# Performance work log

Hardware: AMD Instinct MI355X
Metric: run time of the kernel (lower is better)

## Reference

```python
import jax, jax.numpy as jnp
import numpy as np

B, S, D, H, DFF, HID = 512, 100, 512, 2, 256, 230
DH = D // H


def _ln_torch(x, g, b, eps=1e-5):
    # nn.LayerNorm: biased variance, eps inside sqrt
    m = x.mean(-1, keepdims=True)
    v = ((x - m) ** 2).mean(-1, keepdims=True)
    return g * (x - m) / jnp.sqrt(v + eps) + b


def _ln_custom(x, g, b, eps=1e-6):
    # repo's custom LayerNorm: unbiased std (torch.std default), eps added to std
    m = x.mean(-1, keepdims=True)
    s = jnp.std(x, axis=-1, ddof=1, keepdims=True)
    return g * (x - m) / (s + eps) + b


def setup_inputs() -> dict:
    key = jax.random.key(0)
    ks = jax.random.split(key, 32)
    w = lambda k, shape: jax.random.normal(k, shape, jnp.float32) * 0.02
    return {
        'inp': jax.random.normal(ks[0], (B, S, D), jnp.float32),
        'mask': jax.random.randint(ks[1], (B, S), 0, 2).astype(jnp.int32),
        'gate': jax.random.uniform(ks[2], (B, S, S), jnp.float32),
        'wv': w(ks[3], (D, D)), 'bv': jnp.zeros((D,), jnp.float32),
        'fc_w': w(ks[4], (D, D)), 'fc_b': jnp.zeros((D,), jnp.float32),
        'lnm_g': jnp.ones((D,), jnp.float32), 'lnm_b': jnp.zeros((D,), jnp.float32),
        'w1': w(ks[5], (DFF, D)), 'b1': jnp.zeros((DFF,), jnp.float32),
        'w2': w(ks[6], (D, DFF)), 'b2': jnp.zeros((D,), jnp.float32),
        'lpc_w': w(ks[7], (D, D)), 'lpc_b': jnp.zeros((D,), jnp.float32),
        'lnc_g': jnp.ones((D,), jnp.float32), 'lnc_b': jnp.zeros((D,), jnp.float32),
        'pwf_w': w(ks[8], (DFF, D)), 'pwf_b': jnp.zeros((DFF,), jnp.float32),
        'lpi_w': w(ks[9], (D, DFF)), 'lpi_b': jnp.zeros((D,), jnp.float32),
        'lni_g': jnp.ones((D,), jnp.float32), 'lni_b': jnp.zeros((D,), jnp.float32),
        'lnf_g': jnp.ones((D,), jnp.float32), 'lnf_b': jnp.zeros((D,), jnp.float32),
        'mlpf_w': w(ks[10], (HID, D)), 'mlpf_b': jnp.zeros((HID,), jnp.float32),
    }


def reference(inp, mask, gate, wv, bv, fc_w, fc_b, lnm_g, lnm_b, w1, b1, w2, b2,
              lpc_w, lpc_b, lnc_g, lnc_b, pwf_w, pwf_b, lpi_w, lpi_b,
              lni_g, lni_b, lnf_g, lnf_b, mlpf_w, mlpf_b):
    b = inp.shape[0]
    maskf = mask.astype(jnp.float32)
    masks = maskf[:, :, None] * maskf[:, None, :]              # [B,S,S]
    # In the source, attention scores are FULLY replaced by the mask via
    # torch.where(mask==0, 1e-8, mask); the q/k projections and the gate
    # multiplication have no effect on the output (dead computation).
    attn = jnp.where(masks == 0, jnp.float32(1e-8), masks)
    p = jax.nn.softmax(attn, axis=-1)                          # [B,S,S] (same for both heads)
    v = (inp @ wv.T + bv).reshape(b, S, H, DH)                 # [B,S,H,dh]
    ctx = jnp.einsum('bst,bthd->bshd', p, v).reshape(b, S, D)  # head-concat order matches torch
    mha = _ln_torch(ctx @ fc_w.T + fc_b + inp, lnm_g, lnm_b)   # dropout = identity (eval)
    # 1x1-conv FFN + custom LN
    ffn = jax.nn.relu(mha @ w1.T + b1) @ w2.T + b2
    ctx2 = _ln_custom(ffn + mha, lni_g, lni_b)
    # context projection applied to BOTH original inp and ffn output (shared weights)
    res_inp = _ln_custom((inp @ lpc_w.T + lpc_b) + (ctx2 @ lpc_w.T + lpc_b), lnc_g, lnc_b)
    rv = jax.nn.relu(res_inp @ pwf_w.T + pwf_b) @ lpi_w.T + lpi_b
    res = _ln_custom(rv + res_inp, lnf_g, lnf_b)
    return res @ mlpf_w.T + mlpf_b                             # x_for_att: [B,S,230]
```

## Files before the change

kernel.cpp:

```cpp
#include <hip/hip_runtime.h>

#define BB  512
#define SS  100
#define DD  512
#define DFF 256
#define HIDN 230
#define LDA 520

typedef unsigned short u16;
typedef unsigned int   u32;
typedef __attribute__((ext_vector_type(8))) short v8s;
typedef __attribute__((ext_vector_type(4))) float v4f;

__device__ __forceinline__ float b2f(u16 u){
  union { u32 i; float f; } v; v.i = ((u32)u) << 16; return v.f;
}
__device__ __forceinline__ u16 f2b(float f){
  union { float f; u32 i; } v; v.f = f;
  u32 r = (v.i + 0x7fffu + ((v.i >> 16) & 1u)) >> 16;
  return (u16)r;
}
__device__ __forceinline__ float rsum16(float s){
  #pragma unroll
  for (int o = 1; o < 16; o <<= 1) s += __shfl_xor(s, o, 64);
  return s;
}

template<int K, int NJ>
__device__ __forceinline__ void mm_2m(const u16* __restrict__ a0r,
                                      const u16* __restrict__ a1r,
                                      const u16* __restrict__ b0,
                                      v4f (*acc)[NJ]){
  constexpr int NC = K / 32;
  v8s b[NJ];
  #pragma unroll
  for (int j = 0; j < NJ; j++) b[j] = *(const v8s*)(b0 + (size_t)j*128*K);
  v8s a0 = *(const v8s*)(a0r);
  v8s a1 = *(const v8s*)(a1r);
  #pragma unroll
  for (int kc = 0; kc < NC; kc++){
    v8s bn[NJ]; v8s a0n, a1n;
    if (kc + 1 < NC){
      #pragma unroll
      for (int j = 0; j < NJ; j++)
        bn[j] = *(const v8s*)(b0 + (size_t)j*128*K + (kc+1)*512);
      a0n = *(const v8s*)(a0r + (kc+1)*32);
      a1n = *(const v8s*)(a1r + (kc+1)*32);
    } else {
      #pragma unroll
      for (int j = 0; j < NJ; j++) bn[j] = b[j];
      a0n = a0; a1n = a1;
    }
    #pragma unroll
    for (int j = 0; j < NJ; j++){
      acc[0][j] = __builtin_amdgcn_mfma_f32_16x16x32_bf16(a0, b[j], acc[0][j], 0, 0, 0);
      acc[1][j] = __builtin_amdgcn_mfma_f32_16x16x32_bf16(a1, b[j], acc[1][j], 0, 0, 0);
    }
    #pragma unroll
    for (int j = 0; j < NJ; j++) b[j] = bn[j];
    a0 = a0n; a1 = a1n;
  }
}

template<bool ADDX>
__device__ __forceinline__ void ln_custom_pass(int lrow, int lc,
    const u16 (*src)[LDA], u16 (*dst)[LDA], const u32* xp,
    const u16* __restrict__ g, const u16* __restrict__ bb)
{
  float v[32]; float s = 0.f;
  #pragma unroll
  for (int j = 0; j < 32; j++){ int col = lc + j*16; float x = b2f(src[lrow][col]); v[j] = x; s += x; }
  s = rsum16(s);
  float mean = s * (1.0f/512.0f);
  float vs = 0.f;
  #pragma unroll
  for (int j = 0; j < 32; j++){ float d = v[j] - mean; vs += d*d; }
  vs = rsum16(vs);
  float inv = 1.0f / (sqrtf(vs * (1.0f/511.0f)) + 1e-6f);
  #pragma unroll
  for (int j = 0; j < 32; j++){
    int col = lc + j*16;
    float r = b2f(g[col]) * (v[j] - mean) * inv + b2f(bb[col]);
    if (ADDX){
      u32 p = xp[j >> 1];
      u16 xu = (j & 1) ? (u16)(p >> 16) : (u16)(p & 0xffffu);
      r += b2f(xu);
    }
    dst[lrow][col] = f2b(r);
  }
}

#define NSEG 20
struct CvtArgs {
  const float* src[NSEG];
  u16* dst;
  int off[NSEG];
  int n[NSEG];
  int ncs[6];
  int nin[6];
};
__global__ __launch_bounds__(256) void k_cvt(CvtArgs a){
  int total = a.off[NSEG-1] + a.n[NSEG-1];
  for (int i = blockIdx.x*blockDim.x + threadIdx.x; i < total; i += gridDim.x*blockDim.x){
    int s = 0;
    #pragma unroll
    for (int j = 1; j < NSEG; j++) if (i >= a.off[j]) s = j;
    int o = i - a.off[s];
    if (s < 6){
      int j  = o & 7;
      int l  = (o >> 3) & 63;
      int m  = l & 15, q = l >> 4;
      int rest = o >> 9;
      int ncs = a.ncs[s];
      int kc = rest & ((1 << ncs) - 1);
      int t  = rest >> ncs;
      int col = t*16 + m;
      int k   = kc*32 + q*8 + j;
      int K   = 32 << ncs;
      float v = (col < a.nin[s]) ? a.src[s][(size_t)col*K + k] : 0.f;
      a.dst[i] = f2b(v);
    } else {
      a.dst[i] = f2b(a.src[s][o]);
    }
  }
}

__global__ __launch_bounds__(512) void k_batch(
    const float* __restrict__ inp, const int* __restrict__ mask,
    const float* __restrict__ wv, const float* __restrict__ bv,
    const float* __restrict__ fcw, const float* __restrict__ fcb,
    float* __restrict__ a_m, float* __restrict__ a_u)
{
  __shared__ float sia[DD], sim[DD], cm[DD], cu[DD];
  __shared__ int smask[SS];
  const int b = blockIdx.x, t = threadIdx.x;
  const int lane = t & 63, w8 = t >> 6;
  if (t < SS) smask[t] = mask[b*SS + t];
  __syncthreads();
  const float* base = inp + (size_t)b * SS * DD;
  float aa = 0.f, am = 0.f; int n = 0;
  for (int s = 0; s < SS; s++){
    float x = base[s*DD + t];
    int mk = smask[s];
    aa += x; n += (mk != 0); if (mk) am += x;
  }
  sia[t] = aa; sim[t] = am;
  __syncthreads();
  const float e0 = expf(1e-8f - 1.0f);
  const float denom = (float)n + (float)(SS - n) * e0;
  const float p1 = 1.0f / denom, p0 = e0 / denom;
  {
    float s_a[8], s_m[8];
    #pragma unroll
    for (int j = 0; j < 8; j++){ s_a[j] = sia[lane*8 + j]; s_m[j] = sim[lane*8 + j]; }
    for (int rr = 0; rr < 64; rr++){
      int d = w8*64 + rr;
      const float4* wr = (const float4*)(wv + (size_t)d * DD + lane*8);
      float4 wA = wr[0], wB = wr[1];
      float sva = wA.x*s_a[0] + wA.y*s_a[1] + wA.z*s_a[2] + wA.w*s_a[3]
                + wB.x*s_a[4] + wB.y*s_a[5] + wB.z*s_a[6] + wB.w*s_a[7];
      float svm = wA.x*s_m[0] + wA.y*s_m[1] + wA.z*s_m[2] + wA.w*s_m[3]
                + wB.x*s_m[4] + wB.y*s_m[5] + wB.z*s_m[6] + wB.w*s_m[7];
      #pragma unroll
      for (int o = 1; o < 64; o <<= 1){ sva += __shfl_xor(sva, o, 64); svm += __shfl_xor(svm, o, 64); }
      if (lane == 0){
        float bvd = bv[d];
        sva += (float)SS * bvd;
        svm += (float)n  * bvd;
        cm[d] = p1*svm + p0*(sva - svm);
        cu[d] = sva * (1.0f/(float)SS);
      }
    }
  }
  __syncthreads();
  {
    float c_m[8], c_u[8];
    #pragma unroll
    for (int j = 0; j < 8; j++){ c_m[j] = cm[lane*8 + j]; c_u[j] = cu[lane*8 + j]; }
    for (int rr = 0; rr < 64; rr++){
      int d = w8*64 + rr;
      const float4* fr = (const float4*)(fcw + (size_t)d * DD + lane*8);
      float4 wA = fr[0], wB = fr[1];
      float xm = wA.x*c_m[0] + wA.y*c_m[1] + wA.z*c_m[2] + wA.w*c_m[3]
               + wB.x*c_m[4] + wB.y*c_m[5] + wB.z*c_m[6] + wB.w*c_m[7];
      float xu = wA.x*c_u[0] + wA.y*c_u[1] + wA.z*c_u[2] + wA.w*c_u[3]
               + wB.x*c_u[4] + wB.y*c_u[5] + wB.z*c_u[6] + wB.w*c_u[7];
      #pragma unroll
      for (int o = 1; o < 64; o <<= 1){ xm += __shfl_xor(xm, o, 64); xu += __shfl_xor(xu, o, 64); }
      if (lane == 0){
        float fb = fcb[d];
        a_m[(size_t)b*DD + d] = xm + fb;
        a_u[(size_t)b*DD + d] = xu + fb;
      }
    }
  }
}

__global__ __launch_bounds__(512, 4) void k_main(
    const float* __restrict__ inp, const int* __restrict__ mask,
    const u16* __restrict__ lnm_g, const u16* __restrict__ lnm_b,
    const u16* __restrict__ w1,   const u16* __restrict__ b1,
    const u16* __restrict__ w2,   const u16* __restrict__ b2,
    const u16* __restrict__ lpc_w, const u16* __restrict__ lpc_b,
    const u16* __restrict__ lnc_g, const u16* __restrict__ lnc_b,
    const u16* __restrict__ pwf_w, const u16* __restrict__ pwf_b,
    const u16* __restrict__ lpi_w, const u16* __restrict__ lpi_b,
    const u16* __restrict__ lni_g, const u16* __restrict__ lni_b,
    const u16* __restrict__ lnf_g, const u16* __restrict__ lnf_b,
    const u16* __restrict__ mlpf_w, const u16* __restrict__ mlpf_b,
    const float* __restrict__ a_m, const float* __restrict__ a_u,
    float* __restrict__ out)
{
  __shared__ __align__(16) u16 A[32][LDA];
  __shared__ __align__(16) u16 O[32][LDA];
  __shared__ int marr[32];

  const int tid  = threadIdx.x;
  const int lane = tid & 63, wid = tid >> 6;
  const int m = lane & 15, q = lane >> 4;
  const int r0 = blockIdx.x * 32;
  const int lrow = tid >> 4, lc = tid & 15;

  {
    if (tid < 32) marr[tid] = mask[r0 + tid];
    float4 va[4], vb[4];
    #pragma unroll
    for (int c = 0; c < 4; c++){
      int e = c*4096 + tid*8;
      int row = e >> 9, col = e & 511;
      const float4* p = (const float4*)(inp + (size_t)(r0 + row) * DD + col);
      va[c] = p[0]; vb[c] = p[1];
    }
    #pragma unroll
    for (int c = 0; c < 4; c++){
      int e = c*4096 + tid*8;
      int row = e >> 9, col = e & 511;
      uint4 o;
      o.x = (u32)f2b(va[c].x) | ((u32)f2b(va[c].y) << 16);
      o.y = (u32)f2b(va[c].z) | ((u32)f2b(va[c].w) << 16);
      o.z = (u32)f2b(vb[c].x) | ((u32)f2b(vb[c].y) << 16);
      o.w = (u32)f2b(vb[c].z) | ((u32)f2b(vb[c].w) << 16);
      *(uint4*)&O[row][col] = o;
    }
  }
  __syncthreads();

  u32 xp[16];
  {
    int Rg = r0 + lrow;
    int bi = Rg / SS;
    const float* asel = (marr[lrow] ? a_m : a_u) + (size_t)bi * DD;
    float v[32]; float s = 0.f;
    #pragma unroll
    for (int j = 0; j < 32; j++){
      int col = lc + j*16;
      u16 xu = O[lrow][col];
      if ((j & 1) == 0) xp[j >> 1] = (u32)xu;
      else              xp[j >> 1] |= ((u32)xu << 16);
      float x = asel[col] + b2f(xu);
      v[j] = x; s += x;
    }
    s = rsum16(s);
    float mean = s * (1.0f/512.0f);
    float vs = 0.f;
    #pragma unroll
    for (int j = 0; j < 32; j++){ float d = v[j] - mean; vs += d*d; }
    vs = rsum16(vs);
    float inv = 1.0f / sqrtf(vs * (1.0f/512.0f) + 1e-5f);
    #pragma unroll
    for (int j = 0; j < 32; j++){
      int col = lc + j*16;
      float r = b2f(lnm_g[col]) * (v[j] - mean) * inv + b2f(lnm_b[col]);
      A[lrow][col] = f2b(r);
    }
  }
  __syncthreads();

  {
    v4f acc[2][2];
    #pragma unroll
    for (int mt = 0; mt < 2; mt++)
      #pragma unroll
      for (int j = 0; j < 2; j++) acc[mt][j] = (v4f){0.f,0.f,0.f,0.f};
    mm_2m<512,2>(&A[m][q*8], &A[m+16][q*8], w1 + (size_t)wid*16*512 + lane*8, acc);
    #pragma unroll
    for (int j = 0; j < 2; j++){
      int col = (wid + 8*j)*16 + m;
      float bias = b2f(b1[col]);
      #pragma unroll
      for (int mt = 0; mt < 2; mt++)
        #pragma unroll
        for (int i = 0; i < 4; i++){
          float val = acc[mt][j][i] + bias;
          O[mt*16 + q*4 + i][col] = f2b(val > 0.f ? val : 0.f);
        }
    }
  }
  __syncthreads();

  {
    v4f acc[2][4];
    #pragma unroll
    for (int mt = 0; mt < 2; mt++)
      #pragma unroll
      for (int j = 0; j < 4; j++) acc[mt][j] = (v4f){0.f,0.f,0.f,0.f};
    mm_2m<256,4>(&O[m][q*8], &O[m+16][q*8], w2 + (size_t)wid*16*256 + lane*8, acc);
    __syncthreads();
    #pragma unroll
    for (int j = 0; j < 4; j++){
      int col = (wid + 8*j)*16 + m;
      float bias = b2f(b2[col]);
      #pragma unroll
      for (int mt = 0; mt < 2; mt++)
        #pragma unroll
        for (int i = 0; i < 4; i++){
          int row = mt*16 + q*4 + i;
          O[row][col] = f2b(acc[mt][j][i] + bias + b2f(A[row][col]));
        }
    }
  }
  __syncthreads();

  ln_custom_pass<true>(lrow, lc, O, A, xp, lni_g, lni_b);
  __syncthreads();

  {
    v4f acc[2][4];
    #pragma unroll
    for (int mt = 0; mt < 2; mt++)
      #pragma unroll
      for (int j = 0; j < 4; j++) acc[mt][j] = (v4f){0.f,0.f,0.f,0.f};
    mm_2m<512,4>(&A[m][q*8], &A[m+16][q*8], lpc_w + (size_t)wid*16*512 + lane*8, acc);
    #pragma unroll
    for (int j = 0; j < 4; j++){
      int col = (wid + 8*j)*16 + m;
      float bias = 2.0f * b2f(lpc_b[col]);
      #pragma unroll
      for (int mt = 0; mt < 2; mt++)
        #pragma unroll
        for (int i = 0; i < 4; i++) O[mt*16 + q*4 + i][col] = f2b(acc[mt][j][i] + bias);
    }
  }
  __syncthreads();

  ln_custom_pass<false>(lrow, lc, O, A, nullptr, lnc_g, lnc_b);
  __syncthreads();

  {
    v4f acc[2][2];
    #pragma unroll
    for (int mt = 0; mt < 2; mt++)
      #pragma unroll
      for (int j = 0; j < 2; j++) acc[mt][j] = (v4f){0.f,0.f,0.f,0.f};
    mm_2m<512,2>(&A[m][q*8], &A[m+16][q*8], pwf_w + (size_t)wid*16*512 + lane*8, acc);
    #pragma unroll
    for (int j = 0; j < 2; j++){
      int col = (wid + 8*j)*16 + m;
      float bias = b2f(pwf_b[col]);
      #pragma unroll
      for (int mt = 0; mt < 2; mt++)
        #pragma unroll
        for (int i = 0; i < 4; i++){
          float val = acc[mt][j][i] + bias;
          O[mt*16 + q*4 + i][col] = f2b(val > 0.f ? val : 0.f);
        }
    }
  }
  __syncthreads();

  {
    v4f acc[2][4];
    #pragma unroll
    for (int mt = 0; mt < 2; mt++)
      #pragma unroll
      for (int j = 0; j < 4; j++) acc[mt][j] = (v4f){0.f,0.f,0.f,0.f};
    mm_2m<256,4>(&O[m][q*8], &O[m+16][q*8], lpi_w + (size_t)wid*16*256 + lane*8, acc);
    __syncthreads();
    #pragma unroll
    for (int j = 0; j < 4; j++){
      int col = (wid + 8*j)*16 + m;
      float bias = b2f(lpi_b[col]);
      #pragma unroll
      for (int mt = 0; mt < 2; mt++)
        #pragma unroll
        for (int i = 0; i < 4; i++){
          int row = mt*16 + q*4 + i;
          O[row][col] = f2b(acc[mt][j][i] + bias + b2f(A[row][col]));
        }
    }
  }
  __syncthreads();

  ln_custom_pass<false>(lrow, lc, O, A, nullptr, lnf_g, lnf_b);
  __syncthreads();

  {
    v4f acc[2][2];
    #pragma unroll
    for (int mt = 0; mt < 2; mt++)
      #pragma unroll
      for (int j = 0; j < 2; j++) acc[mt][j] = (v4f){0.f,0.f,0.f,0.f};
    mm_2m<512,2>(&A[m][q*8], &A[m+16][q*8], mlpf_w + (size_t)wid*16*512 + lane*8, acc);
    #pragma unroll
    for (int j = 0; j < 2; j++){
      int col = (wid + 8*j)*16 + m;
      if (col < HIDN){
        float bias = b2f(mlpf_b[col]);
        #pragma unroll
        for (int mt = 0; mt < 2; mt++)
          #pragma unroll
          for (int i = 0; i < 4; i++){
            int row = mt*16 + q*4 + i;
            out[(size_t)(r0 + row)*HIDN + col] = acc[mt][j][i] + bias;
          }
      }
    }
  }
}

extern "C" void kernel_launch(void* const* d_in, const int* in_sizes, int n_in,
                              void* d_out, int out_size, void* d_ws, size_t ws_size,
                              hipStream_t stream)
{
  const float* inp    = (const float*)d_in[0];
  const int*   mask   = (const int*)d_in[1];
  const float* wv     = (const float*)d_in[3];
  const float* bv     = (const float*)d_in[4];
  const float* fc_w   = (const float*)d_in[5];
  const float* fc_b   = (const float*)d_in[6];

  float* a_m = (float*)d_ws;
  float* a_u = a_m + (size_t)BB * DD;
  u16* bfb = (u16*)((char*)d_ws + 2u * BB * DD * sizeof(float));

  const int OW1   = 0;
  const int OW2   = OW1   + DFF*DD;
  const int OLPC  = OW2   + DD*DFF;
  const int OPWF  = OLPC  + DD*DD;
  const int OLPI  = OPWF  + DFF*DD;
  const int OMLPF = OLPI  + DD*DFF;
  int voff = OMLPF + 256*DD;
  const int OLNMG = voff; voff += DD;
  const int OLNMB = voff; voff += DD;
  const int OB1   = voff; voff += DFF;
  const int OB2   = voff; voff += DD;
  const int OLPCB = voff; voff += DD;
  const int OLNCG = voff; voff += DD;
  const int OLNCB = voff; voff += DD;
  const int OPWFB = voff; voff += DFF;
  const int OLPIB = voff; voff += DD;
  const int OLNIG = voff; voff += DD;
  const int OLNIB = voff; voff += DD;
  const int OLNFG = voff; voff += DD;
  const int OLNFB = voff; voff += DD;
  const int OMLPFB = voff; voff += HIDN;

  CvtArgs ca;
  const int srcidx[NSEG] = {9, 11, 13, 17, 19, 25,
                            7, 8, 10, 12, 14, 15, 16, 18, 20, 21, 22, 23, 24, 26};
  const int offs[NSEG]   = {OW1, OW2, OLPC, OPWF, OLPI, OMLPF,
                            OLNMG, OLNMB, OB1, OB2, OLPCB, OLNCG, OLNCB, OPWFB,
                            OLPIB, OLNIG, OLNIB, OLNFG, OLNFB, OMLPFB};
  const int lens[NSEG]   = {DFF*DD, DD*DFF, DD*DD, DFF*DD, DD*DFF, 256*DD,
                            DD, DD, DFF, DD, DD, DD, DD, DFF, DD, DD, DD, DD, DD, HIDN};
  const int ncss[6] = {4, 3, 4, 4, 3, 4};
  const int nins[6] = {DFF, DD, DD, DFF, DD, HIDN};
  for (int i = 0; i < NSEG; i++){
    ca.src[i] = (const float*)d_in[srcidx[i]];
    ca.off[i] = offs[i];
    ca.n[i]   = lens[i];
  }
  for (int i = 0; i < 6; i++){ ca.ncs[i] = ncss[i]; ca.nin[i] = nins[i]; }
  ca.dst = bfb;

  k_cvt<<<512, 256, 0, stream>>>(ca);
  k_batch<<<BB, 512, 0, stream>>>(inp, mask, wv, bv, fc_w, fc_b, a_m, a_u);
  k_main<<<(BB*SS)/32, 512, 0, stream>>>(inp, mask,
      bfb + OLNMG, bfb + OLNMB,
      bfb + OW1,   bfb + OB1,
      bfb + OW2,   bfb + OB2,
      bfb + OLPC,  bfb + OLPCB,
      bfb + OLNCG, bfb + OLNCB,
      bfb + OPWF,  bfb + OPWFB,
      bfb + OLPI,  bfb + OLPIB,
      bfb + OLNIG, bfb + OLNIB,
      bfb + OLNFG, bfb + OLNFB,
      bfb + OMLPF, bfb + OMLPFB,
      a_m, a_u, (float*)d_out);
}
```

Before: 588.0 us.

## Process 64 rows per block with 16 waves and fuse conversion into prep kernel

New measurement: 540.3 us. -8.1%, faster.

```diff
diff --git a/kernel.cpp b/kernel.cpp
--- a/kernel.cpp
+++ b/kernel.cpp
@@ -26,39 +26,41 @@
   return s;
 }
 
-template<int K, int NJ>
-__device__ __forceinline__ void mm_2m(const u16* __restrict__ a0r,
-                                      const u16* __restrict__ a1r,
-                                      const u16* __restrict__ b0,
-                                      v4f (*acc)[NJ]){
+template<int K, int NT>
+__device__ __forceinline__ void mm64(const u16 (*Asrc)[LDA], const u16* __restrict__ W,
+                                     int w, int lane, int m, int q, v4f (*acc)[NT]){
   constexpr int NC = K / 32;
-  v8s b[NJ];
-  #pragma unroll
-  for (int j = 0; j < NJ; j++) b[j] = *(const v8s*)(b0 + (size_t)j*128*K);
-  v8s a0 = *(const v8s*)(a0r);
-  v8s a1 = *(const v8s*)(a1r);
+  const u16* b0 = W + (size_t)w*16*K + lane*8;
+  v8s a[4], b[NT];
+  #pragma unroll
+  for (int mt = 0; mt < 4; mt++) a[mt] = *(const v8s*)(&Asrc[mt*16 + m][q*8]);
+  #pragma unroll
+  for (int j = 0; j < NT; j++)  b[j]  = *(const v8s*)(b0 + (size_t)j*256*K);
   #pragma unroll
   for (int kc = 0; kc < NC; kc++){
-    v8s bn[NJ]; v8s a0n, a1n;
+    v8s an[4], bn[NT];
     if (kc + 1 < NC){
       #pragma unroll
-      for (int j = 0; j < NJ; j++)
-        bn[j] = *(const v8s*)(b0 + (size_t)j*128*K + (kc+1)*512);
-      a0n = *(const v8s*)(a0r + (kc+1)*32);
-      a1n = *(const v8s*)(a1r + (kc+1)*32);
+      for (int j = 0; j < NT; j++)
+        bn[j] = *(const v8s*)(b0 + (size_t)j*256*K + (kc+1)*512);
+      #pragma unroll
+      for (int mt = 0; mt < 4; mt++)
+        an[mt] = *(const v8s*)(&Asrc[mt*16 + m][(kc+1)*32 + q*8]);
     } else {
       #pragma unroll
-      for (int j = 0; j < NJ; j++) bn[j] = b[j];
-      a0n = a0; a1n = a1;
-    }
-    #pragma unroll
-    for (int j = 0; j < NJ; j++){
-      acc[0][j] = __builtin_amdgcn_mfma_f32_16x16x32_bf16(a0, b[j], acc[0][j], 0, 0, 0);
-      acc[1][j] = __builtin_amdgcn_mfma_f32_16x16x32_bf16(a1, b[j], acc[1][j], 0, 0, 0);
-    }
-    #pragma unroll
-    for (int j = 0; j < NJ; j++) b[j] = bn[j];
-    a0 = a0n; a1 = a1n;
+      for (int j = 0; j < NT; j++) bn[j] = b[j];
+      #pragma unroll
+      for (int mt = 0; mt < 4; mt++) an[mt] = a[mt];
+    }
+    #pragma unroll
+    for (int j = 0; j < NT; j++)
+      #pragma unroll
+      for (int mt = 0; mt < 4; mt++)
+        acc[mt][j] = __builtin_amdgcn_mfma_f32_16x16x32_bf16(a[mt], b[j], acc[mt][j], 0, 0, 0);
+    #pragma unroll
+    for (int j = 0; j < NT; j++) b[j] = bn[j];
+    #pragma unroll
+    for (int mt = 0; mt < 4; mt++) a[mt] = an[mt];
   }
 }
 
@@ -99,38 +101,37 @@
   int ncs[6];
   int nin[6];
 };
-__global__ __launch_bounds__(256) void k_cvt(CvtArgs a){
-  int total = a.off[NSEG-1] + a.n[NSEG-1];
-  for (int i = blockIdx.x*blockDim.x + threadIdx.x; i < total; i += gridDim.x*blockDim.x){
-    int s = 0;
-    #pragma unroll
-    for (int j = 1; j < NSEG; j++) if (i >= a.off[j]) s = j;
-    int o = i - a.off[s];
-    if (s < 6){
-      int j  = o & 7;
-      int l  = (o >> 3) & 63;
-      int m  = l & 15, q = l >> 4;
-      int rest = o >> 9;
-      int ncs = a.ncs[s];
-      int kc = rest & ((1 << ncs) - 1);
-      int t  = rest >> ncs;
-      int col = t*16 + m;
-      int k   = kc*32 + q*8 + j;
-      int K   = 32 << ncs;
-      float v = (col < a.nin[s]) ? a.src[s][(size_t)col*K + k] : 0.f;
-      a.dst[i] = f2b(v);
-    } else {
-      a.dst[i] = f2b(a.src[s][o]);
-    }
-  }
-}
-
-__global__ __launch_bounds__(512) void k_batch(
+__global__ __launch_bounds__(512) void k_pre(CvtArgs a,
     const float* __restrict__ inp, const int* __restrict__ mask,
     const float* __restrict__ wv, const float* __restrict__ bv,
     const float* __restrict__ fcw, const float* __restrict__ fcb,
     float* __restrict__ a_m, float* __restrict__ a_u)
 {
+  {
+    int total = a.off[NSEG-1] + a.n[NSEG-1];
+    for (int i = blockIdx.x*blockDim.x + threadIdx.x; i < total; i += gridDim.x*blockDim.x){
+      int s = 0;
+      #pragma unroll
+      for (int j = 1; j < NSEG; j++) if (i >= a.off[j]) s = j;
+      int o = i - a.off[s];
+      if (s < 6){
+        int j  = o & 7;
+        int l  = (o >> 3) & 63;
+        int m  = l & 15, q = l >> 4;
+        int rest = o >> 9;
+        int ncs = a.ncs[s];
+        int kc = rest & ((1 << ncs) - 1);
+        int t  = rest >> ncs;
+        int col = t*16 + m;
+        int k   = kc*32 + q*8 + j;
+        int K   = 32 << ncs;
+        float v = (col < a.nin[s]) ? a.src[s][(size_t)col*K + k] : 0.f;
+        a.dst[i] = f2b(v);
+      } else {
+        a.dst[i] = f2b(a.src[s][o]);
+      }
+    }
+  }
   __shared__ float sia[DD], sim[DD], cm[DD], cu[DD];
   __shared__ int smask[SS];
   const int b = blockIdx.x, t = threadIdx.x;
@@ -196,7 +197,7 @@
   }
 }
 
-__global__ __launch_bounds__(512, 4) void k_main(
+__global__ __launch_bounds__(1024, 4) void k_main(
     const float* __restrict__ inp, const int* __restrict__ mask,
     const u16* __restrict__ lnm_g, const u16* __restrict__ lnm_b,
     const u16* __restrict__ w1,   const u16* __restrict__ b1,
@@ -211,29 +212,29 @@
     const float* __restrict__ a_m, const float* __restrict__ a_u,
     float* __restrict__ out)
 {
-  __shared__ __align__(16) u16 A[32][LDA];
-  __shared__ __align__(16) u16 O[32][LDA];
-  __shared__ int marr[32];
+  __shared__ __align__(16) u16 A[64][LDA];
+  __shared__ __align__(16) u16 O[64][LDA];
+  __shared__ int marr[64];
 
   const int tid  = threadIdx.x;
   const int lane = tid & 63, wid = tid >> 6;
   const int m = lane & 15, q = lane >> 4;
-  const int r0 = blockIdx.x * 32;
+  const int r0 = blockIdx.x * 64;
   const int lrow = tid >> 4, lc = tid & 15;
 
   {
-    if (tid < 32) marr[tid] = mask[r0 + tid];
+    if (tid < 64) marr[tid] = mask[r0 + tid];
     float4 va[4], vb[4];
     #pragma unroll
     for (int c = 0; c < 4; c++){
-      int e = c*4096 + tid*8;
+      int e = c*8192 + tid*8;
       int row = e >> 9, col = e & 511;
       const float4* p = (const float4*)(inp + (size_t)(r0 + row) * DD + col);
       va[c] = p[0]; vb[c] = p[1];
     }
     #pragma unroll
     for (int c = 0; c < 4; c++){
-      int e = c*4096 + tid*8;
+      int e = c*8192 + tid*8;
       int row = e >> 9, col = e & 511;
       uint4 o;
       o.x = (u32)f2b(va[c].x) | ((u32)f2b(va[c].y) << 16);
@@ -277,41 +278,36 @@
   __syncthreads();
 
   {
-    v4f acc[2][2];
-    #pragma unroll
-    for (int mt = 0; mt < 2; mt++)
+    v4f acc[4][1];
+    #pragma unroll
+    for (int mt = 0; mt < 4; mt++) acc[mt][0] = (v4f){0.f,0.f,0.f,0.f};
+    mm64<512,1>(A, w1, wid, lane, m, q, acc);
+    int col = wid*16 + m;
+    float bias = b2f(b1[col]);
+    #pragma unroll
+    for (int mt = 0; mt < 4; mt++)
+      #pragma unroll
+      for (int i = 0; i < 4; i++){
+        float val = acc[mt][0][i] + bias;
+        O[mt*16 + q*4 + i][col] = f2b(val > 0.f ? val : 0.f);
+      }
+  }
+  __syncthreads();
+
+  {
+    v4f acc[4][2];
+    #pragma unroll
+    for (int mt = 0; mt < 4; mt++)
       #pragma unroll
       for (int j = 0; j < 2; j++) acc[mt][j] = (v4f){0.f,0.f,0.f,0.f};
-    mm_2m<512,2>(&A[m][q*8], &A[m+16][q*8], w1 + (size_t)wid*16*512 + lane*8, acc);
+    mm64<256,2>(O, w2, wid, lane, m, q, acc);
+    __syncthreads();
     #pragma unroll
     for (int j = 0; j < 2; j++){
-      int col = (wid + 8*j)*16 + m;
-      float bias = b2f(b1[col]);
-      #pragma unroll
-      for (int mt = 0; mt < 2; mt++)
-        #pragma unroll
-        for (int i = 0; i < 4; i++){
-          float val = acc[mt][j][i] + bias;
-          O[mt*16 + q*4 + i][col] = f2b(val > 0.f ? val : 0.f);
-        }
-    }
-  }
-  __syncthreads();
-
-  {
-    v4f acc[2][4];
-    #pragma unroll
-    for (int mt = 0; mt < 2; mt++)
-      #pragma unroll
-      for (int j = 0; j < 4; j++) acc[mt][j] = (v4f){0.f,0.f,0.f,0.f};
-    mm_2m<256,4>(&O[m][q*8], &O[m+16][q*8], w2 + (size_t)wid*16*256 + lane*8, acc);
-    __syncthreads();
-    #pragma unroll
-    for (int j = 0; j < 4; j++){
-      int col = (wid + 8*j)*16 + m;
+      int col = (wid + 16*j)*16 + m;
       float bias = b2f(b2[col]);
       #pragma unroll
-      for (int mt = 0; mt < 2; mt++)
+      for (int mt = 0; mt < 4; mt++)
         #pragma unroll
         for (int i = 0; i < 4; i++){
           int row = mt*16 + q*4 + i;
@@ -325,18 +321,18 @@
   __syncthreads();
 
   {
-    v4f acc[2][4];
-    #pragma unroll
-    for (int mt = 0; mt < 2; mt++)
-      #pragma unroll
-      for (int j = 0; j < 4; j++) acc[mt][j] = (v4f){0.f,0.f,0.f,0.f};
-    mm_2m<512,4>(&A[m][q*8], &A[m+16][q*8], lpc_w + (size_t)wid*16*512 + lane*8, acc);
-    #pragma unroll
-    for (int j = 0; j < 4; j++){
-      int col = (wid + 8*j)*16 + m;
+    v4f acc[4][2];
+    #pragma unroll
+    for (int mt = 0; mt < 4; mt++)
+      #pragma unroll
+      for (int j = 0; j < 2; j++) acc[mt][j] = (v4f){0.f,0.f,0.f,0.f};
+    mm64<512,2>(A, lpc_w, wid, lane, m, q, acc);
+    #pragma unroll
+    for (int j = 0; j < 2; j++){
+      int col = (wid + 16*j)*16 + m;
       float bias = 2.0f * b2f(lpc_b[col]);
       #pragma unroll
-      for (int mt = 0; mt < 2; mt++)
+      for (int mt = 0; mt < 4; mt++)
         #pragma unroll
         for (int i = 0; i < 4; i++) O[mt*16 + q*4 + i][col] = f2b(acc[mt][j][i] + bias);
     }
@@ -347,41 +343,36 @@
   __syncthreads();
 
   {
-    v4f acc[2][2];
-    #pragma unroll
-    for (int mt = 0; mt < 2; mt++)
+    v4f acc[4][1];
+    #pragma unroll
+    for (int mt = 0; mt < 4; mt++) acc[mt][0] = (v4f){0.f,0.f,0.f,0.f};
+    mm64<512,1>(A, pwf_w, wid, lane, m, q, acc);
+    int col = wid*16 + m;
+    float bias = b2f(pwf_b[col]);
+    #pragma unroll
+    for (int mt = 0; mt < 4; mt++)
+      #pragma unroll
+      for (int i = 0; i < 4; i++){
+        float val = acc[mt][0][i] + bias;
+        O[mt*16 + q*4 + i][col] = f2b(val > 0.f ? val : 0.f);
+      }
+  }
+  __syncthreads();
+
+  {
+    v4f acc[4][2];
+    #pragma unroll
+    for (int mt = 0; mt < 4; mt++)
       #pragma unroll
       for (int j = 0; j < 2; j++) acc[mt][j] = (v4f){0.f,0.f,0.f,0.f};
-    mm_2m<512,2>(&A[m][q*8], &A[m+16][q*8], pwf_w + (size_t)wid*16*512 + lane*8, acc);
+    mm64<256,2>(O, lpi_w, wid, lane, m, q, acc);
+    __syncthreads();
     #pragma unroll
     for (int j = 0; j < 2; j++){
-      int col = (wid + 8*j)*16 + m;
-      float bias = b2f(pwf_b[col]);
-      #pragma unroll
-      for (int mt = 0; mt < 2; mt++)
-        #pragma unroll
-        for (int i = 0; i < 4; i++){
-          float val = acc[mt][j][i] + bias;
-          O[mt*16 + q*4 + i][col] = f2b(val > 0.f ? val : 0.f);
-        }
-    }
-  }
-  __syncthreads();
-
-  {
-    v4f acc[2][4];
-    #pragma unroll
-    for (int mt = 0; mt < 2; mt++)
-      #pragma unroll
-      for (int j = 0; j < 4; j++) acc[mt][j] = (v4f){0.f,0.f,0.f,0.f};
-    mm_2m<256,4>(&O[m][q*8], &O[m+16][q*8], lpi_w + (size_t)wid*16*256 + lane*8, acc);
-    __syncthreads();
-    #pragma unroll
-    for (int j = 0; j < 4; j++){
-      int col = (wid + 8*j)*16 + m;
+      int col = (wid + 16*j)*16 + m;
       float bias = b2f(lpi_b[col]);
       #pragma unroll
-      for (int mt = 0; mt < 2; mt++)
+      for (int mt = 0; mt < 4; mt++)
         #pragma unroll
         for (int i = 0; i < 4; i++){
           int row = mt*16 + q*4 + i;
@@ -395,25 +386,20 @@
   __syncthreads();
 
   {
-    v4f acc[2][2];
-    #pragma unroll
-    for (int mt = 0; mt < 2; mt++)
-      #pragma unroll
-      for (int j = 0; j < 2; j++) acc[mt][j] = (v4f){0.f,0.f,0.f,0.f};
-    mm_2m<512,2>(&A[m][q*8], &A[m+16][q*8], mlpf_w + (size_t)wid*16*512 + lane*8, acc);
-    #pragma unroll
-    for (int j = 0; j < 2; j++){
-      int col = (wid + 8*j)*16 + m;
-      if (col < HIDN){
-        float bias = b2f(mlpf_b[col]);
+    v4f acc[4][1];
+    #pragma unroll
+    for (int mt = 0; mt < 4; mt++) acc[mt][0] = (v4f){0.f,0.f,0.f,0.f};
+    mm64<512,1>(A, mlpf_w, wid, lane, m, q, acc);
+    int col = wid*16 + m;
+    if (col < HIDN){
+      float bias = b2f(mlpf_b[col]);
+      #pragma unroll
+      for (int mt = 0; mt < 4; mt++)
         #pragma unroll
-        for (int mt = 0; mt < 2; mt++)
-          #pragma unroll
-          for (int i = 0; i < 4; i++){
-            int row = mt*16 + q*4 + i;
-            out[(size_t)(r0 + row)*HIDN + col] = acc[mt][j][i] + bias;
-          }
-      }
+        for (int i = 0; i < 4; i++){
+          int row = mt*16 + q*4 + i;
+          out[(size_t)(r0 + row)*HIDN + col] = acc[mt][0][i] + bias;
+        }
     }
   }
 }
@@ -473,9 +459,8 @@
   for (int i = 0; i < 6; i++){ ca.ncs[i] = ncss[i]; ca.nin[i] = nins[i]; }
   ca.dst = bfb;
 
-  k_cvt<<<512, 256, 0, stream>>>(ca);
-  k_batch<<<BB, 512, 0, stream>>>(inp, mask, wv, bv, fc_w, fc_b, a_m, a_u);
-  k_main<<<(BB*SS)/32, 512, 0, stream>>>(inp, mask,
+  k_pre<<<BB, 512, 0, stream>>>(ca, inp, mask, wv, bv, fc_w, fc_b, a_m, a_u);
+  k_main<<<(BB*SS)/64, 1024, 0, stream>>>(inp, mask,
       bfb + OLNMG, bfb + OLNMB,
       bfb + OW1,   bfb + OB1,
       bfb + OW2,   bfb + OB2,
```

## Merge conversion into batch kernel and shrink shared memory with in-place LN buffers

Applied to the files above, without the earlier changes.

After: 577.0 us. Within noise of the previous version (-1.9%).

```diff
diff --git a/kernel.cpp b/kernel.cpp
--- a/kernel.cpp
+++ b/kernel.cpp
@@ -6,6 +6,7 @@
 #define DFF 256
 #define HIDN 230
 #define LDA 520
+#define LDB 264
 
 typedef unsigned short u16;
 typedef unsigned int   u32;
@@ -26,50 +27,52 @@
   return s;
 }
 
-template<int K, int NJ>
-__device__ __forceinline__ void mm_2m(const u16* __restrict__ a0r,
-                                      const u16* __restrict__ a1r,
-                                      const u16* __restrict__ b0,
-                                      v4f (*acc)[NJ]){
+template<int K, int NT, int LDAS>
+__device__ __forceinline__ void mmW(const u16 (*Asrc)[LDAS], const u16* __restrict__ W,
+                                    int w, int lane, int m, int q, v4f (*acc)[NT]){
   constexpr int NC = K / 32;
-  v8s b[NJ];
-  #pragma unroll
-  for (int j = 0; j < NJ; j++) b[j] = *(const v8s*)(b0 + (size_t)j*128*K);
-  v8s a0 = *(const v8s*)(a0r);
-  v8s a1 = *(const v8s*)(a1r);
+  const u16* b0 = W + (size_t)w*16*K + lane*8;
+  v8s a[2], b[NT];
+  #pragma unroll
+  for (int mt = 0; mt < 2; mt++) a[mt] = *(const v8s*)(&Asrc[mt*16 + m][q*8]);
+  #pragma unroll
+  for (int j = 0; j < NT; j++)  b[j]  = *(const v8s*)(b0 + (size_t)j*128*K);
   #pragma unroll
   for (int kc = 0; kc < NC; kc++){
-    v8s bn[NJ]; v8s a0n, a1n;
+    v8s an[2], bn[NT];
     if (kc + 1 < NC){
       #pragma unroll
-      for (int j = 0; j < NJ; j++)
+      for (int j = 0; j < NT; j++)
         bn[j] = *(const v8s*)(b0 + (size_t)j*128*K + (kc+1)*512);
-      a0n = *(const v8s*)(a0r + (kc+1)*32);
-      a1n = *(const v8s*)(a1r + (kc+1)*32);
+      #pragma unroll
+      for (int mt = 0; mt < 2; mt++)
+        an[mt] = *(const v8s*)(&Asrc[mt*16 + m][(kc+1)*32 + q*8]);
     } else {
       #pragma unroll
-      for (int j = 0; j < NJ; j++) bn[j] = b[j];
-      a0n = a0; a1n = a1;
-    }
-    #pragma unroll
-    for (int j = 0; j < NJ; j++){
-      acc[0][j] = __builtin_amdgcn_mfma_f32_16x16x32_bf16(a0, b[j], acc[0][j], 0, 0, 0);
-      acc[1][j] = __builtin_amdgcn_mfma_f32_16x16x32_bf16(a1, b[j], acc[1][j], 0, 0, 0);
-    }
-    #pragma unroll
-    for (int j = 0; j < NJ; j++) b[j] = bn[j];
-    a0 = a0n; a1 = a1n;
+      for (int j = 0; j < NT; j++) bn[j] = b[j];
+      #pragma unroll
+      for (int mt = 0; mt < 2; mt++) an[mt] = a[mt];
+    }
+    #pragma unroll
+    for (int j = 0; j < NT; j++)
+      #pragma unroll
+      for (int mt = 0; mt < 2; mt++)
+        acc[mt][j] = __builtin_amdgcn_mfma_f32_16x16x32_bf16(a[mt], b[j], acc[mt][j], 0, 0, 0);
+    #pragma unroll
+    for (int j = 0; j < NT; j++) b[j] = bn[j];
+    #pragma unroll
+    for (int mt = 0; mt < 2; mt++) a[mt] = an[mt];
   }
 }
 
 template<bool ADDX>
-__device__ __forceinline__ void ln_custom_pass(int lrow, int lc,
-    const u16 (*src)[LDA], u16 (*dst)[LDA], const u32* xp,
+__device__ __forceinline__ void ln_custom_ip(int lrow, int lc,
+    u16 (*buf)[LDA], const u32* xp,
     const u16* __restrict__ g, const u16* __restrict__ bb)
 {
   float v[32]; float s = 0.f;
   #pragma unroll
-  for (int j = 0; j < 32; j++){ int col = lc + j*16; float x = b2f(src[lrow][col]); v[j] = x; s += x; }
+  for (int j = 0; j < 32; j++){ int col = lc + j*16; float x = b2f(buf[lrow][col]); v[j] = x; s += x; }
   s = rsum16(s);
   float mean = s * (1.0f/512.0f);
   float vs = 0.f;
@@ -86,7 +89,7 @@
       u16 xu = (j & 1) ? (u16)(p >> 16) : (u16)(p & 0xffffu);
       r += b2f(xu);
     }
-    dst[lrow][col] = f2b(r);
+    buf[lrow][col] = f2b(r);
   }
 }
 
@@ -99,38 +102,37 @@
   int ncs[6];
   int nin[6];
 };
-__global__ __launch_bounds__(256) void k_cvt(CvtArgs a){
-  int total = a.off[NSEG-1] + a.n[NSEG-1];
-  for (int i = blockIdx.x*blockDim.x + threadIdx.x; i < total; i += gridDim.x*blockDim.x){
-    int s = 0;
-    #pragma unroll
-    for (int j = 1; j < NSEG; j++) if (i >= a.off[j]) s = j;
-    int o = i - a.off[s];
-    if (s < 6){
-      int j  = o & 7;
-      int l  = (o >> 3) & 63;
-      int m  = l & 15, q = l >> 4;
-      int rest = o >> 9;
-      int ncs = a.ncs[s];
-      int kc = rest & ((1 << ncs) - 1);
-      int t  = rest >> ncs;
-      int col = t*16 + m;
-      int k   = kc*32 + q*8 + j;
-      int K   = 32 << ncs;
-      float v = (col < a.nin[s]) ? a.src[s][(size_t)col*K + k] : 0.f;
-      a.dst[i] = f2b(v);
-    } else {
-      a.dst[i] = f2b(a.src[s][o]);
-    }
-  }
-}
-
-__global__ __launch_bounds__(512) void k_batch(
+__global__ __launch_bounds__(512) void k_pre(CvtArgs a,
     const float* __restrict__ inp, const int* __restrict__ mask,
     const float* __restrict__ wv, const float* __restrict__ bv,
     const float* __restrict__ fcw, const float* __restrict__ fcb,
     float* __restrict__ a_m, float* __restrict__ a_u)
 {
+  {
+    int total = a.off[NSEG-1] + a.n[NSEG-1];
+    for (int i = blockIdx.x*blockDim.x + threadIdx.x; i < total; i += gridDim.x*blockDim.x){
+      int s = 0;
+      #pragma unroll
+      for (int j = 1; j < NSEG; j++) if (i >= a.off[j]) s = j;
+      int o = i - a.off[s];
+      if (s < 6){
+        int j  = o & 7;
+        int l  = (o >> 3) & 63;
+        int m  = l & 15, q = l >> 4;
+        int rest = o >> 9;
+        int ncs = a.ncs[s];
+        int kc = rest & ((1 << ncs) - 1);
+        int t  = rest >> ncs;
+        int col = t*16 + m;
+        int k   = kc*32 + q*8 + j;
+        int K   = 32 << ncs;
+        float v = (col < a.nin[s]) ? a.src[s][(size_t)col*K + k] : 0.f;
+        a.dst[i] = f2b(v);
+      } else {
+        a.dst[i] = f2b(a.src[s][o]);
+      }
+    }
+  }
   __shared__ float sia[DD], sim[DD], cm[DD], cu[DD];
   __shared__ int smask[SS];
   const int b = blockIdx.x, t = threadIdx.x;
@@ -196,7 +198,7 @@
   }
 }
 
-__global__ __launch_bounds__(512, 4) void k_main(
+__global__ __launch_bounds__(512, 1) void k_main(
     const float* __restrict__ inp, const int* __restrict__ mask,
     const u16* __restrict__ lnm_g, const u16* __restrict__ lnm_b,
     const u16* __restrict__ w1,   const u16* __restrict__ b1,
@@ -211,8 +213,8 @@
     const float* __restrict__ a_m, const float* __restrict__ a_u,
     float* __restrict__ out)
 {
-  __shared__ __align__(16) u16 A[32][LDA];
-  __shared__ __align__(16) u16 O[32][LDA];
+  __shared__ __align__(16) u16 B1[32][LDA];
+  __shared__ __align__(16) u16 B2[32][LDB];
   __shared__ int marr[32];
 
   const int tid  = threadIdx.x;
@@ -240,7 +242,7 @@
       o.y = (u32)f2b(va[c].z) | ((u32)f2b(va[c].w) << 16);
       o.z = (u32)f2b(vb[c].x) | ((u32)f2b(vb[c].y) << 16);
       o.w = (u32)f2b(vb[c].z) | ((u32)f2b(vb[c].w) << 16);
-      *(uint4*)&O[row][col] = o;
+      *(uint4*)&B1[row][col] = o;
     }
   }
   __syncthreads();
@@ -254,7 +256,7 @@
     #pragma unroll
     for (int j = 0; j < 32; j++){
       int col = lc + j*16;
-      u16 xu = O[lrow][col];
+      u16 xu = B1[lrow][col];
       if ((j & 1) == 0) xp[j >> 1] = (u32)xu;
       else              xp[j >> 1] |= ((u32)xu << 16);
       float x = asel[col] + b2f(xu);
@@ -271,7 +273,7 @@
     for (int j = 0; j < 32; j++){
       int col = lc + j*16;
       float r = b2f(lnm_g[col]) * (v[j] - mean) * inv + b2f(lnm_b[col]);
-      A[lrow][col] = f2b(r);
+      B1[lrow][col] = f2b(r);
     }
   }
   __syncthreads();
@@ -282,7 +284,7 @@
     for (int mt = 0; mt < 2; mt++)
       #pragma unroll
       for (int j = 0; j < 2; j++) acc[mt][j] = (v4f){0.f,0.f,0.f,0.f};
-    mm_2m<512,2>(&A[m][q*8], &A[m+16][q*8], w1 + (size_t)wid*16*512 + lane*8, acc);
+    mmW<512,2,LDA>(B1, w1, wid, lane, m, q, acc);
     #pragma unroll
     for (int j = 0; j < 2; j++){
       int col = (wid + 8*j)*16 + m;
@@ -292,7 +294,7 @@
         #pragma unroll
         for (int i = 0; i < 4; i++){
           float val = acc[mt][j][i] + bias;
-          O[mt*16 + q*4 + i][col] = f2b(val > 0.f ? val : 0.f);
+          B2[mt*16 + q*4 + i][col] = f2b(val > 0.f ? val : 0.f);
         }
     }
   }
@@ -304,8 +306,7 @@
     for (int mt = 0; mt < 2; mt++)
       #pragma unroll
       for (int j = 0; j < 4; j++) acc[mt][j] = (v4f){0.f,0.f,0.f,0.f};
-    mm_2m<256,4>(&O[m][q*8], &O[m+16][q*8], w2 + (size_t)wid*16*256 + lane*8, acc);
-    __syncthreads();
+    mmW<256,4,LDB>(B2, w2, wid, lane, m, q, acc);
     #pragma unroll
     for (int j = 0; j < 4; j++){
       int col = (wid + 8*j)*16 + m;
@@ -315,13 +316,13 @@
         #pragma unroll
         for (int i = 0; i < 4; i++){
           int row = mt*16 + q*4 + i;
-          O[row][col] = f2b(acc[mt][j][i] + bias + b2f(A[row][col]));
+          B1[row][col] = f2b(acc[mt][j][i] + bias + b2f(B1[row][col]));
         }
     }
   }
   __syncthreads();
 
-  ln_custom_pass<true>(lrow, lc, O, A, xp, lni_g, lni_b);
+  ln_custom_ip<true>(lrow, lc, B1, xp, lni_g, lni_b);
   __syncthreads();
 
   {
@@ -330,7 +331,8 @@
     for (int mt = 0; mt < 2; mt++)
       #pragma unroll
       for (int j = 0; j < 4; j++) acc[mt][j] = (v4f){0.f,0.f,0.f,0.f};
-    mm_2m<512,4>(&A[m][q*8], &A[m+16][q*8], lpc_w + (size_t)wid*16*512 + lane*8, acc);
+    mmW<512,4,LDA>(B1, lpc_w, wid, lane, m, q, acc);
+    __syncthreads();
     #pragma unroll
     for (int j = 0; j < 4; j++){
       int col = (wid + 8*j)*16 + m;
@@ -338,12 +340,12 @@
       #pragma unroll
       for (int mt = 0; mt < 2; mt++)
         #pragma unroll
-        for (int i = 0; i < 4; i++) O[mt*16 + q*4 + i][col] = f2b(acc[mt][j][i] + bias);
-    }
-  }
-  __syncthreads();
-
-  ln_custom_pass<false>(lrow, lc, O, A, nullptr, lnc_g, lnc_b);
+        for (int i = 0; i < 4; i++) B1[mt*16 + q*4 + i][col] = f2b(acc[mt][j][i] + bias);
+    }
+  }
+  __syncthreads();
+
+  ln_custom_ip<false>(lrow, lc, B1, nullptr, lnc_g, lnc_b);
   __syncthreads();
 
   {
@@ -352,7 +354,7 @@
     for (int mt = 0; mt < 2; mt++)
       #pragma unroll
       for (int j = 0; j < 2; j++) acc[mt][j] = (v4f){0.f,0.f,0.f,0.f};
-    mm_2m<512,2>(&A[m][q*8], &A[m+16][q*8], pwf_w + (size_t)wid*16*512 + lane*8, acc);
+    mmW<512,2,LDA>(B1, pwf_w, wid, lane, m, q, acc);
     #pragma unroll
     for (int j = 0; j < 2; j++){
       int col = (wid + 8*j)*16 + m;
@@ -362,7 +364,7 @@
         #pragma unroll
         for (int i = 0; i < 4; i++){
           float val = acc[mt][j][i] + bias;
-          O[mt*16 + q*4 + i][col] = f2b(val > 0.f ? val : 0.f);
+          B2[mt*16 + q*4 + i][col] = f2b(val > 0.f ? val : 0.f);
         }
     }
   }
@@ -374,8 +376,7 @@
     for (int mt = 0; mt < 2; mt++)
       #pragma unroll
       for (int j = 0; j < 4; j++) acc[mt][j] = (v4f){0.f,0.f,0.f,0.f};
-    mm_2m<256,4>(&O[m][q*8], &O[m+16][q*8], lpi_w + (size_t)wid*16*256 + lane*8, acc);
-    __syncthreads();
+    mmW<256,4,LDB>(B2, lpi_w, wid, lane, m, q, acc);
     #pragma unroll
     for (int j = 0; j < 4; j++){
       int col = (wid + 8*j)*16 + m;
@@ -385,13 +386,13 @@
         #pragma unroll
         for (int i = 0; i < 4; i++){
           int row = mt*16 + q*4 + i;
-          O[row][col] = f2b(acc[mt][j][i] + bias + b2f(A[row][col]));
+          B1[row][col] = f2b(acc[mt][j][i] + bias + b2f(B1[row][col]));
         }
     }
   }
   __syncthreads();
 
-  ln_custom_pass<false>(lrow, lc, O, A, nullptr, lnf_g, lnf_b);
+  ln_custom_ip<false>(lrow, lc, B1, nullptr, lnf_g, lnf_b);
   __syncthreads();
 
   {
@@ -400,7 +401,7 @@
     for (int mt = 0; mt < 2; mt++)
       #pragma unroll
       for (int j = 0; j < 2; j++) acc[mt][j] = (v4f){0.f,0.f,0.f,0.f};
-    mm_2m<512,2>(&A[m][q*8], &A[m+16][q*8], mlpf_w + (size_t)wid*16*512 + lane*8, acc);
+    mmW<512,2,LDA>(B1, mlpf_w, wid, lane, m, q, acc);
     #pragma unroll
     for (int j = 0; j < 2; j++){
       int col = (wid + 8*j)*16 + m;
@@ -473,8 +474,7 @@
   for (int i = 0; i < 6; i++){ ca.ncs[i] = ncss[i]; ca.nin[i] = nins[i]; }
   ca.dst = bfb;
 
-  k_cvt<<<512, 256, 0, stream>>>(ca);
-  k_batch<<<BB, 512, 0, stream>>>(inp, mask, wv, bv, fc_w, fc_b, a_m, a_u);
+  k_pre<<<BB, 512, 0, stream>>>(ca, inp, mask, wv, bv, fc_w, fc_b, a_m, a_u);
   k_main<<<(BB*SS)/32, 512, 0, stream>>>(inp, mask,
       bfb + OLNMG, bfb + OLNMB,
       bfb + OW1,   bfb + OB1,
```
